# Performance work log

Measured on AMD Instinct MI355X. Metric: run time of the kernel, lower is better.

Reference implementation:

```python
import jax, jax.numpy as jnp
import numpy as np

SCALING = 32.0 / 16.0  # alpha / r

def setup_inputs() -> dict:
    key = jax.random.key(0)
    k1, k2, k3, k4 = jax.random.split(key, 4)
    B_, S, D_in, D_out, R = 4, 2048, 4096, 4096, 16
    x = jax.random.normal(k1, (B_, S, D_in), dtype=jnp.float32)
    W_base = jax.random.normal(k2, (D_out, D_in), dtype=jnp.float32) * 0.02
    b_base = jax.random.normal(k3, (D_out,), dtype=jnp.float32) * 0.02
    A = jax.random.normal(k4, (R, D_in), dtype=jnp.float32) * 0.02
    B = jnp.zeros((D_out, R), dtype=jnp.float32)  # lora_B init to zeros
    return {"x": x, "W_base": W_base, "b_base": b_base, "A": A, "B": B}

def reference(x, W_base, b_base, A, B):
    # base linear (stands in for dequantized 4-bit matmul): [B,S,Din] @ [Din,Dout]
    out = jnp.einsum('bsd,od->bso', x, W_base) + b_base
    # LoRA path: B(A(x)) * scaling, dropout=0 -> identity
    xa = jnp.einsum('bsd,rd->bsr', x, A)        # [B,S,r]
    delta = jnp.einsum('bsr,or->bso', xa, B)    # [B,S,Dout]
    return out + delta * SCALING
```

## Files before the change

### kernel.cpp

```cpp
#include <hip/hip_runtime.h>


typedef __attribute__((ext_vector_type(4))) float f32x4;
typedef __attribute__((ext_vector_type(8))) short bf16x8;

__device__ __forceinline__ unsigned short f2bf(float f) {
    unsigned u = __builtin_bit_cast(unsigned, f);
    unsigned r = u + 0x7fffu + ((u >> 16) & 1u);
    return (unsigned short)(r >> 16);
}

__device__ __forceinline__ void gload_lds16(const void* g, void* l) {
    __builtin_amdgcn_global_load_lds(
        (const __attribute__((address_space(1))) void*)g,
        (__attribute__((address_space(3))) void*)l, 16, 0, 0);
}

__global__ __launch_bounds__(256) void cast_x_kernel(
    const float* __restrict__ x, unsigned short* __restrict__ xb, int n8)
{
    int stride = gridDim.x * blockDim.x;
    for (int i = blockIdx.x * blockDim.x + threadIdx.x; i < n8; i += stride) {
        size_t base = (size_t)i * 8;
        float4 f0 = *(const float4*)&x[base];
        float4 f1 = *(const float4*)&x[base + 4];
        ushort4 o0, o1;
        o0.x = f2bf(f0.x); o0.y = f2bf(f0.y); o0.z = f2bf(f0.z); o0.w = f2bf(f0.w);
        o1.x = f2bf(f1.x); o1.y = f2bf(f1.y); o1.z = f2bf(f1.z); o1.w = f2bf(f1.w);
        *(ushort4*)&xb[base]     = o0;
        *(ushort4*)&xb[base + 4] = o1;
    }
}

__global__ __launch_bounds__(256) void prep_w_kernel(
    const float* __restrict__ W, const float* __restrict__ A,
    const float* __restrict__ Bl, unsigned short* __restrict__ wb,
    int K, float scale)
{
    __shared__ float Bs[16][16];
    const int t = threadIdx.x;
    const int n0 = blockIdx.y * 16;
    const int k0 = blockIdx.x * 256;
    {
        int nl = t >> 4, r = t & 15;
        Bs[nl][r] = Bl[(size_t)(n0 + nl) * 16 + r];
    }
    __syncthreads();

    const int lane = t & 63;
    const int wv = t >> 6;
    const int k = k0 + lane * 4;

    float4 av[16];
#pragma unroll
    for (int r = 0; r < 16; ++r)
        av[r] = *(const float4*)&A[(size_t)r * K + k];

#pragma unroll
    for (int j = 0; j < 4; ++j) {
        const int nl = wv * 4 + j;
        const int n = n0 + nl;
        float4 w = *(const float4*)&W[(size_t)n * K + k];
        float d0 = 0.f, d1 = 0.f, d2 = 0.f, d3 = 0.f;
#pragma unroll
        for (int r = 0; r < 16; ++r) {
            float b = Bs[nl][r];
            d0 += b * av[r].x; d1 += b * av[r].y;
            d2 += b * av[r].z; d3 += b * av[r].w;
        }
        ushort4 o;
        o.x = f2bf(w.x + scale * d0);
        o.y = f2bf(w.y + scale * d1);
        o.z = f2bf(w.z + scale * d2);
        o.w = f2bf(w.w + scale * d3);
        *(ushort4*)&wb[(size_t)n * K + k] = o;
    }
}


#define SETPRIO(p) __builtin_amdgcn_s_setprio(p)
#define BARRIER()  __builtin_amdgcn_s_barrier()
#define LGKM0()    asm volatile("s_waitcnt lgkmcnt(0)" ::: "memory")

__global__ __launch_bounds__(512, 2) void gemm256_kernel(
    const unsigned short* __restrict__ Xb, const unsigned short* __restrict__ Wb,
    const float* __restrict__ bias, float* __restrict__ out,
    int M, int N, int K)
{
    __shared__ __align__(16) unsigned short lds[2][2][2][8192];

    const int NT = K / 64;
    const int ntn = N / 256;
    int bid = blockIdx.x;
    {
        int per = gridDim.x >> 3;
        bid = (bid & 7) * per + (bid >> 3);
    }
    const int tm = bid / ntn, tn = bid % ntn;

    const int t = threadIdx.x;
    const int lane = t & 63, wave = t >> 6;
    const int wr = wave >> 2;
    const int wc = wave & 3;
    const int wch = wc >> 1;
    const int bro = (wc & 1) * 64;

    const int srow = t >> 3;
    const int scol = ((t & 7) * 8) ^ (((t >> 3) & 7) << 3);
    unsigned gA[2][2], gB[2][2];
#pragma unroll
    for (int h = 0; h < 2; ++h)
#pragma unroll
        for (int i = 0; i < 2; ++i) {
            gA[h][i] = (unsigned)((tm * 256 + h * 128 + i * 64 + srow) * K + scol);
            gB[h][i] = (unsigned)((tn * 256 + h * 128 + i * 64 + srow) * K + scol);
        }

#define ST_A4(buf, ktt)                                                         \
    _Pragma("unroll") for (int h = 0; h < 2; ++h)                               \
    _Pragma("unroll") for (int i = 0; i < 2; ++i)                               \
        gload_lds16(Xb + gA[h][i] + (ktt) * 64,                                 \
                    &lds[buf][0][h][i * 4096 + wave * 512]);
#define ST_B4(buf, ktt)                                                         \
    _Pragma("unroll") for (int h = 0; h < 2; ++h)                               \
    _Pragma("unroll") for (int i = 0; i < 2; ++i)                               \
        gload_lds16(Wb + gB[h][i] + (ktt) * 64,                                 \
                    &lds[buf][1][h][i * 4096 + wave * 512]);

    const int fr = lane & 15;
    const int hi16 = ((lane >> 4) & 3) * 16;
    const int bsw = (fr & 7) << 4;
    const int lo0 = hi16 ^ bsw;
    const int lo1 = (64 + hi16) ^ bsw;

    f32x4 acc[8][4] = {};
    bf16x8 a03[4][2], a47[4][2], b01[2][2], b23[2][2];

#define RD_A03(P)                                                               \
    _Pragma("unroll") for (int i = 0; i < 4; ++i) {                             \
        a03[i][0] = *(const bf16x8*)((P) + (i * 16 + fr) * 128 + lo0);          \
        a03[i][1] = *(const bf16x8*)((P) + (i * 16 + fr) * 128 + lo1);          \
    }
#define RD_A47(P)                                                               \
    _Pragma("unroll") for (int i = 0; i < 4; ++i) {                             \
        a47[i][0] = *(const bf16x8*)((P) + ((4 + i) * 16 + fr) * 128 + lo0);    \
        a47[i][1] = *(const bf16x8*)((P) + ((4 + i) * 16 + fr) * 128 + lo1);    \
    }
#define RD_B01(P)                                                               \
    _Pragma("unroll") for (int i = 0; i < 2; ++i) {                             \
        b01[i][0] = *(const bf16x8*)((P) + (bro + i * 16 + fr) * 128 + lo0);    \
        b01[i][1] = *(const bf16x8*)((P) + (bro + i * 16 + fr) * 128 + lo1);    \
    }
#define RD_B23(P)                                                               \
    _Pragma("unroll") for (int i = 0; i < 2; ++i) {                             \
        b23[i][0] = *(const bf16x8*)((P) + (bro + (2+i) * 16 + fr) * 128 + lo0);\
        b23[i][1] = *(const bf16x8*)((P) + (bro + (2+i) * 16 + fr) * 128 + lo1);\
    }

#define MFMA_Q(AV, BV, M0, N0)                                                  \
    _Pragma("unroll") for (int kk = 0; kk < 2; ++kk)                            \
    _Pragma("unroll") for (int mi = 0; mi < 4; ++mi)                            \
    _Pragma("unroll") for (int ni = 0; ni < 2; ++ni)                            \
        acc[(M0) + mi][(N0) + ni] = __builtin_amdgcn_mfma_f32_16x16x32_bf16(    \
            AV[mi][kk], BV[ni][kk], acc[(M0) + mi][(N0) + ni], 0, 0, 0);

    ST_A4(0, 0) ST_B4(0, 0)
    ST_A4(1, 1) ST_B4(1, 1)
    asm volatile("s_waitcnt vmcnt(8)" ::: "memory");
    BARRIER();
    {
        const char* pA = (const char*)&lds[0][0][wr][0];
        const char* pB = (const char*)&lds[0][1][wch][0];
        RD_A03(pA)
        RD_B01(pB)
    }

    for (int kt = 0; kt < NT; ++kt) {
        const int cur = kt & 1;
        const char* pA  = (const char*)&lds[cur][0][wr][0];
        const char* pB  = (const char*)&lds[cur][1][wch][0];
        const char* pA1 = (const char*)&lds[cur ^ 1][0][wr][0];
        const char* pB1 = (const char*)&lds[cur ^ 1][1][wch][0];
        const bool stB = (kt + 1 < NT);
        const bool stA = (kt + 2 < NT);

        LGKM0();
        RD_A47(pA)
        SETPRIO(1);
        MFMA_Q(a03, b01, 0, 0)
        SETPRIO(0);
        BARRIER();

        LGKM0();
        RD_B23(pB)
        SETPRIO(1);
        MFMA_Q(a47, b01, 4, 0)
        SETPRIO(0);
        asm volatile("s_waitcnt vmcnt(0)" ::: "memory");
        BARRIER();

        LGKM0();
        if (stB) { RD_B01(pB1) }
        if (stA) { ST_A4(cur, kt + 2) }
        SETPRIO(1);
        MFMA_Q(a03, b23, 0, 2)
        SETPRIO(0);
        BARRIER();

        if (stB) { RD_A03(pA1) }
        if (stA) { ST_B4(cur, kt + 2) }
        SETPRIO(1);
        MFMA_Q(a47, b23, 4, 2)
        SETPRIO(0);
        BARRIER();
    }

    const int row0 = tm * 256 + wr * 128 + (lane >> 4) * 4;
    const int col0 = tn * 256 + wc * 64;
#pragma unroll
    for (int ni = 0; ni < 4; ++ni) {
        const int col = col0 + ni * 16 + fr;
        const float bv = bias[col];
#pragma unroll
        for (int mi = 0; mi < 8; ++mi) {
            const int row = row0 + mi * 16;
#pragma unroll
            for (int r = 0; r < 4; ++r)
                out[(size_t)(row + r) * N + col] = acc[mi][ni][r] + bv;
        }
    }
}

extern "C" void kernel_launch(void* const* d_in, const int* in_sizes, int n_in,
                              void* d_out, int out_size, void* d_ws, size_t ws_size,
                              hipStream_t stream)
{
    const float* x  = (const float*)d_in[0];
    const float* W  = (const float*)d_in[1];
    const float* b  = (const float*)d_in[2];
    const float* A  = (const float*)d_in[3];
    const float* Bl = (const float*)d_in[4];
    float* out = (float*)d_out;

    const int Dout = in_sizes[2];
    const int Din  = in_sizes[1] / Dout;
    const int M    = in_sizes[0] / Din;

    unsigned short* xb = (unsigned short*)d_ws;
    unsigned short* wb = xb + (size_t)M * Din;

    dim3 gw(Din / 256, Dout / 16);
    prep_w_kernel<<<gw, 256, 0, stream>>>(W, A, Bl, wb, Din, 2.0f);

    cast_x_kernel<<<2048, 256, 0, stream>>>(x, xb, M * Din / 8);

    const int grid = (M / 256) * (Dout / 256);
    gemm256_kernel<<<grid, 512, 0, stream>>>(xb, wb, b, out, M, Dout, Din);
}
```

Measured before the change: 296.8 us.

## Make GEMM blocks process two M-tiles, overlapping next-tile prefetch with epilogue

Each workgroup now computes two 256x256 output tiles that share a column tile, one after the other, and the grid is halved. The first prologue loads of the second tile are issued before the first tile's epilogue stores, so global loads overlap the output writes and launch/prologue costs are amortised. The row offset of 16 tiles is hardcoded (it assumes M/256 = 32) and halving the grid reduces parallelism to 256 blocks, which may leave CUs underused on a 256-CU device.

```diff
diff --git a/kernel.cpp b/kernel.cpp
--- a/kernel.cpp
+++ b/kernel.cpp
@@ -96,7 +96,8 @@
         int per = gridDim.x >> 3;
         bid = (bid & 7) * per + (bid >> 3);
     }
-    const int tm = bid / ntn, tn = bid % ntn;
+    const int tm0 = bid / ntn;
+    const int tn  = bid % ntn;
 
     const int t = threadIdx.x;
     const int lane = t & 63, wave = t >> 6;
@@ -112,8 +113,8 @@
     for (int h = 0; h < 2; ++h)
 #pragma unroll
         for (int i = 0; i < 2; ++i) {
-            gA[h][i] = (unsigned)((tm * 256 + h * 128 + i * 64 + srow) * K + scol);
-            gB[h][i] = (unsigned)((tn * 256 + h * 128 + i * 64 + srow) * K + scol);
+            gA[h][i] = (unsigned)((tm0 * 256 + h * 128 + i * 64 + srow) * K + scol);
+            gB[h][i] = (unsigned)((tn  * 256 + h * 128 + i * 64 + srow) * K + scol);
         }
 
 #define ST_A4(buf, ktt)                                                         \
@@ -133,7 +134,12 @@
     const int lo0 = hi16 ^ bsw;
     const int lo1 = (64 + hi16) ^ bsw;
 
-    f32x4 acc[8][4] = {};
+    const f32x4 zero4 = {0.f, 0.f, 0.f, 0.f};
+    f32x4 acc[8][4];
+#pragma unroll
+    for (int mi = 0; mi < 8; ++mi)
+#pragma unroll
+        for (int ni = 0; ni < 4; ++ni) acc[mi][ni] = zero4;
     bf16x8 a03[4][2], a47[4][2], b01[2][2], b23[2][2];
 
 #define RD_A03(P)                                                               \
@@ -175,58 +181,86 @@
         RD_B01(pB)
     }
 
-    for (int kt = 0; kt < NT; ++kt) {
-        const int cur = kt & 1;
-        const char* pA  = (const char*)&lds[cur][0][wr][0];
-        const char* pB  = (const char*)&lds[cur][1][wch][0];
-        const char* pA1 = (const char*)&lds[cur ^ 1][0][wr][0];
-        const char* pB1 = (const char*)&lds[cur ^ 1][1][wch][0];
-        const bool stB = (kt + 1 < NT);
-        const bool stA = (kt + 2 < NT);
-
-        LGKM0();
-        RD_A47(pA)
-        SETPRIO(1);
-        MFMA_Q(a03, b01, 0, 0)
-        SETPRIO(0);
-        BARRIER();
-
-        LGKM0();
-        RD_B23(pB)
-        SETPRIO(1);
-        MFMA_Q(a47, b01, 4, 0)
-        SETPRIO(0);
-        asm volatile("s_waitcnt vmcnt(0)" ::: "memory");
-        BARRIER();
-
-        LGKM0();
-        if (stB) { RD_B01(pB1) }
-        if (stA) { ST_A4(cur, kt + 2) }
-        SETPRIO(1);
-        MFMA_Q(a03, b23, 0, 2)
-        SETPRIO(0);
-        BARRIER();
-
-        if (stB) { RD_A03(pA1) }
-        if (stA) { ST_B4(cur, kt + 2) }
-        SETPRIO(1);
-        MFMA_Q(a47, b23, 4, 2)
-        SETPRIO(0);
-        BARRIER();
-    }
-
-    const int row0 = tm * 256 + wr * 128 + (lane >> 4) * 4;
     const int col0 = tn * 256 + wc * 64;
-#pragma unroll
-    for (int ni = 0; ni < 4; ++ni) {
-        const int col = col0 + ni * 16 + fr;
-        const float bv = bias[col];
-#pragma unroll
-        for (int mi = 0; mi < 8; ++mi) {
-            const int row = row0 + mi * 16;
-#pragma unroll
-            for (int r = 0; r < 4; ++r)
-                out[(size_t)(row + r) * N + col] = acc[mi][ni][r] + bv;
+
+#pragma unroll 1
+    for (int rep = 0; rep < 2; ++rep) {
+        for (int kt = 0; kt < NT; ++kt) {
+            const int cur = kt & 1;
+            const char* pA  = (const char*)&lds[cur][0][wr][0];
+            const char* pB  = (const char*)&lds[cur][1][wch][0];
+            const char* pA1 = (const char*)&lds[cur ^ 1][0][wr][0];
+            const char* pB1 = (const char*)&lds[cur ^ 1][1][wch][0];
+            const bool stB = (kt + 1 < NT);
+            const bool stA = (kt + 2 < NT);
+
+            LGKM0();
+            RD_A47(pA)
+            SETPRIO(1);
+            MFMA_Q(a03, b01, 0, 0)
+            SETPRIO(0);
+            BARRIER();
+
+            LGKM0();
+            RD_B23(pB)
+            SETPRIO(1);
+            MFMA_Q(a47, b01, 4, 0)
+            SETPRIO(0);
+            asm volatile("s_waitcnt vmcnt(0)" ::: "memory");
+            BARRIER();
+
+            LGKM0();
+            if (stB) { RD_B01(pB1) }
+            if (stA) { ST_A4(cur, kt + 2) }
+            SETPRIO(1);
+            MFMA_Q(a03, b23, 0, 2)
+            SETPRIO(0);
+            BARRIER();
+
+            if (stB) { RD_A03(pA1) }
+            if (stA) { ST_B4(cur, kt + 2) }
+            SETPRIO(1);
+            MFMA_Q(a47, b23, 4, 2)
+            SETPRIO(0);
+            BARRIER();
+        }
+
+        const int row0 = (tm0 + rep * 16) * 256 + wr * 128 + (lane >> 4) * 4;
+
+        if (rep == 0) {
+#pragma unroll
+            for (int h = 0; h < 2; ++h)
+#pragma unroll
+                for (int i = 0; i < 2; ++i)
+                    gA[h][i] += (unsigned)(16 * 256) * (unsigned)K;
+            ST_A4(0, 0) ST_B4(0, 0)
+            ST_A4(1, 1) ST_B4(1, 1)
+        }
+
+#pragma unroll
+        for (int ni = 0; ni < 4; ++ni) {
+            const int col = col0 + ni * 16 + fr;
+            const float bv = bias[col];
+#pragma unroll
+            for (int mi = 0; mi < 8; ++mi) {
+                const int row = row0 + mi * 16;
+#pragma unroll
+                for (int r = 0; r < 4; ++r)
+                    out[(size_t)(row + r) * N + col] = acc[mi][ni][r] + bv;
+            }
+        }
+
+        if (rep == 0) {
+            asm volatile("s_waitcnt vmcnt(0)" ::: "memory");
+            BARRIER();
+            const char* pA = (const char*)&lds[0][0][wr][0];
+            const char* pB = (const char*)&lds[0][1][wch][0];
+            RD_A03(pA)
+            RD_B01(pB)
+#pragma unroll
+            for (int mi = 0; mi < 8; ++mi)
+#pragma unroll
+                for (int ni = 0; ni < 4; ++ni) acc[mi][ni] = zero4;
         }
     }
 }
@@ -254,6 +288,6 @@
 
     cast_x_kernel<<<2048, 256, 0, stream>>>(x, xb, M * Din / 8);
 
-    const int grid = (M / 256) * (Dout / 256);
+    const int grid = (M / 256) * (Dout / 256) / 2;
     gemm256_kernel<<<grid, 512, 0, stream>>>(xb, wb, b, out, M, Dout, Din);
 }
```

After: 301.4 us. No clear change (+1.5%).
